# Optimization experiments

Hardware: AMD Instinct MI355X
Metric: run time of the kernel (lower is better)

Reference implementation:

```python
import jax, jax.numpy as jnp
import numpy as np
from jax import lax

NUM_GROUP = 512
GROUP_SIZE = 32


def fps(xyz, npoint):
    """Farthest point sampling. xyz: [B, N, 3] -> centers [B, npoint, 3]."""
    B, N, _ = xyz.shape
    big = jnp.asarray(1e10, xyz.dtype)

    def body(carry, _):
        min_d, farthest = carry  # [B, N], [B]
        centroid = jnp.take_along_axis(xyz, farthest[:, None, None], axis=1)  # [B,1,3]
        d = jnp.sum((xyz - centroid) ** 2, axis=-1)  # [B, N]
        min_d = jnp.minimum(min_d, d)
        nxt = jnp.argmax(min_d, axis=-1).astype(jnp.int32)
        return (min_d, nxt), farthest

    init = (jnp.full((B, N), big, xyz.dtype), jnp.zeros((B,), jnp.int32))
    _, idxs = lax.scan(body, init, None, length=npoint)  # [npoint, B]
    idxs = idxs.T  # [B, npoint]
    return jnp.take_along_axis(xyz, idxs[..., None], axis=1)  # [B, npoint, 3]


def knn_idx(xyz, center, k):
    """xyz [B,N,3], center [B,G,3] -> idx [B,G,k] of k nearest (squared L2)."""
    # [B, G, N] squared distances
    d2 = jnp.sum((center[:, :, None, :] - xyz[:, None, :, :]) ** 2, axis=-1)
    _, idx = lax.top_k(-d2, k)  # smallest distances
    return idx


def setup_inputs() -> dict:
    key = jax.random.key(0)
    xyz = jax.random.normal(key, (32, 3, 8192), dtype=jnp.float32)
    return {"xyz": xyz}


def reference(xyz):
    # xyz: [B, 3, N] -> [B, N, 3]
    pts = jnp.transpose(xyz, (0, 2, 1))[:, :, :3]
    B, N, _ = pts.shape
    center = fps(pts, NUM_GROUP)                  # [B, G, 3]
    idx = knn_idx(pts, center, GROUP_SIZE)        # [B, G, k]
    flat_idx = idx.reshape(B, NUM_GROUP * GROUP_SIZE)
    neighborhood = jnp.take_along_axis(pts, flat_idx[..., None], axis=1)
    neighborhood = neighborhood.reshape(B, NUM_GROUP, GROUP_SIZE, 3)
    neighborhood = neighborhood - center[:, :, None, :]
    return neighborhood, center
```

## Files before the change

kernel.cpp:

```cpp
#include <hip/hip_runtime.h>

typedef unsigned long long u64;
typedef unsigned int u32;
typedef float v2f __attribute__((ext_vector_type(2)));

#define BATCH 32
#define NPTS  8192
#define NGRP  512
#define KNN_K 32

#define FPS_T 256
#define FPS_W (FPS_T / 64)
#define PPAIR (NPTS / FPS_T / 2)
#define KNN_WPB 4
#define QCAP 128

__device__ __forceinline__ float sq3(float dx, float dy, float dz) {
    return __fadd_rn(__fadd_rn(__fmul_rn(dx, dx), __fmul_rn(dy, dy)), __fmul_rn(dz, dz));
}

__device__ __forceinline__ u64 packdi(float d, int n) {
    return ((u64)__float_as_uint(d) << 32) | (u32)n;
}

__device__ __forceinline__ u64 umin64(u64 a, u64 b) { return a < b ? a : b; }
__device__ __forceinline__ u64 umax64(u64 a, u64 b) { return a > b ? a : b; }

__device__ __forceinline__ u64 shfl_xor_u64(u64 v, int m) {
    int lo = __shfl_xor((int)(u32)v, m, 64);
    int hi = __shfl_xor((int)(u32)(v >> 32), m, 64);
    return ((u64)(u32)hi << 32) | (u32)lo;
}

__device__ __forceinline__ u64 shfl_u64(u64 v, int src) {
    int lo = __shfl((int)(u32)v, src, 64);
    int hi = __shfl((int)(u32)(v >> 32), src, 64);
    return ((u64)(u32)hi << 32) | (u32)lo;
}

template <int CTRL>
__device__ __forceinline__ u64 dpp_max_step(u64 k) {
    u32 plo = (u32)__builtin_amdgcn_update_dpp(0, (int)(u32)k, CTRL, 0xF, 0xF, true);
    u32 phi = (u32)__builtin_amdgcn_update_dpp(0, (int)(u32)(k >> 32), CTRL, 0xF, 0xF, true);
    u64 p = ((u64)phi << 32) | plo;
    return k > p ? k : p;
}
__device__ __forceinline__ u64 dpp_wave_max(u64 k) {
    k = dpp_max_step<0x111>(k);
    k = dpp_max_step<0x112>(k);
    k = dpp_max_step<0x114>(k);
    k = dpp_max_step<0x118>(k);
    k = dpp_max_step<0x142>(k);
    k = dpp_max_step<0x143>(k);
    return k;
}

__device__ __forceinline__ u64 lane_sort64(u64 v, int lane) {
#pragma unroll
    for (int k = 2; k <= 64; k <<= 1) {
#pragma unroll
        for (int j = k >> 1; j > 0; j >>= 1) {
            u64 p = shfl_xor_u64(v, j);
            bool keepmin = (((lane & k) == 0) == ((lane & j) == 0));
            u64 mn = umin64(v, p), mx = umax64(v, p);
            v = keepmin ? mn : mx;
        }
    }
    return v;
}

__device__ __forceinline__ u64 lane_merge64(u64 m, u64 c, int lane) {
    u64 cr = shfl_xor_u64(c, 63);
    u64 z = umin64(m, cr);
#pragma unroll
    for (int dd = 32; dd > 0; dd >>= 1) {
        u64 p = shfl_xor_u64(z, dd);
        u64 mn = umin64(z, p), mx = umax64(z, p);
        z = (lane & dd) ? mx : mn;
    }
    return z;
}

__device__ __forceinline__ void knn_step(u64& m, u64& tau, int& cnt, u64* sbuf,
                                         float x, float y, float z,
                                         float cx, float cy, float cz,
                                         int n, int lane) {
    float d = sq3(__fsub_rn(x, cx), __fsub_rn(y, cy), __fsub_rn(z, cz));
    u64 kk = packdi(d, n);
    bool cand = kk < tau;
    u64 mask = __ballot(cand);
    if (mask) {
        u32 below = __builtin_amdgcn_mbcnt_hi(
            (u32)(mask >> 32), __builtin_amdgcn_mbcnt_lo((u32)mask, 0));
        if (cand) sbuf[cnt + below] = kk;
        cnt += (int)__popcll(mask);
        if (cnt >= 64) {
            u64 c = sbuf[lane];
            c = lane_sort64(c, lane);
            m = lane_merge64(m, c, lane);
            tau = shfl_u64(m, 31);
            int rem = cnt - 64;
            if (lane < rem) sbuf[lane] = sbuf[64 + lane];
            cnt = rem;
        }
    }
}

__global__ __launch_bounds__(FPS_T) void fps_kernel(const float* __restrict__ in,
                                                    float* __restrict__ centers) {
#pragma clang fp contract(off)
    __shared__ float sx[NPTS];
    __shared__ float sy[NPTS];
    __shared__ float sz[NPTS];
    __shared__ u64 s_key[2][FPS_W];
    __shared__ float s_out[NGRP * 3];

    const int b = blockIdx.x;
    const int t = threadIdx.x;
    const int w = t >> 6;
    const float* xp = in + (size_t)b * 3 * NPTS;
    const float* yp = xp + NPTS;
    const float* zp = xp + 2 * NPTS;

    v2f xr[PPAIR], yr[PPAIR], zr[PPAIR], md[PPAIR];
#pragma unroll
    for (int i = 0; i < PPAIR; ++i) {
        int n = i * (2 * FPS_T) + 2 * t;
        xr[i] = *(const v2f*)(xp + n);
        yr[i] = *(const v2f*)(yp + n);
        zr[i] = *(const v2f*)(zp + n);
        *(v2f*)(sx + n) = xr[i];
        *(v2f*)(sy + n) = yr[i];
        *(v2f*)(sz + n) = zr[i];
        md[i] = (v2f){1e10f, 1e10f};
    }
    __syncthreads();

    int cur = 0;
    for (int r = 0; r < NGRP; ++r) {
        const float cx = sx[cur], cy = sy[cur], cz = sz[cur];
        if (t == 0) {
            s_out[r * 3 + 0] = cx;
            s_out[r * 3 + 1] = cy;
            s_out[r * 3 + 2] = cz;
        }

        float bd0 = -1.0f, bd1 = -1.0f;
        int   bi0 = 0,     bi1 = 0;
#pragma unroll
        for (int i = 0; i < PPAIR; ++i) {
            v2f dx = xr[i] - cx;
            v2f dy = yr[i] - cy;
            v2f dz = zr[i] - cz;
            v2f dd = dx * dx + dy * dy + dz * dz;
            md[i] = __builtin_elementwise_min(md[i], dd);
            int n = i * (2 * FPS_T) + 2 * t;
            if (md[i].x > bd0) { bd0 = md[i].x; bi0 = n; }
            if (md[i].y > bd1) { bd1 = md[i].y; bi1 = n + 1; }
        }
        u64 k0 = ((u64)__float_as_uint(bd0) << 32) | (u32)(~(u32)bi0);
        u64 k1 = ((u64)__float_as_uint(bd1) << 32) | (u32)(~(u32)bi1);
        u64 k = dpp_wave_max(umax64(k0, k1));
        if ((t & 63) == 63) s_key[r & 1][w] = k;
        __syncthreads();
        u64 m = umax64(umax64(s_key[r & 1][0], s_key[r & 1][1]),
                       umax64(s_key[r & 1][2], s_key[r & 1][3]));
        cur = (int)(~(u32)m);
    }

    __syncthreads();
    float* cdst = centers + (size_t)b * NGRP * 3;
    for (int i = t; i < NGRP * 3; i += FPS_T) cdst[i] = s_out[i];
}

__global__ __launch_bounds__(KNN_WPB * 64) void knn_kernel(const float* __restrict__ in,
                                                           const float* __restrict__ centers,
                                                           float* __restrict__ out) {
    __shared__ u64 sbuf[KNN_WPB][QCAP];

    const int wave = threadIdx.x >> 6;
    const int lane = threadIdx.x & 63;
    const int cid  = blockIdx.x * KNN_WPB + wave;
    const int b    = cid >> 9;

    const float* xp = in + (size_t)b * 3 * NPTS;
    const float* yp = xp + NPTS;
    const float* zp = xp + 2 * NPTS;

    const float cx = centers[cid * 3 + 0];
    const float cy = centers[cid * 3 + 1];
    const float cz = centers[cid * 3 + 2];

    float x = xp[lane], y = yp[lane], z = zp[lane];
    u64 m = packdi(sq3(__fsub_rn(x, cx), __fsub_rn(y, cy), __fsub_rn(z, cz)), lane);
    m = lane_sort64(m, lane);
    u64 tau = shfl_u64(m, 31);
    int cnt = 0;

    int j = 1;
#pragma unroll 1
    for (; j + 3 < NPTS / 64; j += 4) {
        int n0 = j * 64 + lane, n1 = n0 + 64, n2 = n0 + 128, n3 = n0 + 192;
        float x0 = xp[n0], y0 = yp[n0], z0 = zp[n0];
        float x1 = xp[n1], y1 = yp[n1], z1 = zp[n1];
        float x2 = xp[n2], y2 = yp[n2], z2 = zp[n2];
        float x3 = xp[n3], y3 = yp[n3], z3 = zp[n3];
        knn_step(m, tau, cnt, sbuf[wave], x0, y0, z0, cx, cy, cz, n0, lane);
        knn_step(m, tau, cnt, sbuf[wave], x1, y1, z1, cx, cy, cz, n1, lane);
        knn_step(m, tau, cnt, sbuf[wave], x2, y2, z2, cx, cy, cz, n2, lane);
        knn_step(m, tau, cnt, sbuf[wave], x3, y3, z3, cx, cy, cz, n3, lane);
    }
    for (; j < NPTS / 64; ++j) {
        int n = j * 64 + lane;
        knn_step(m, tau, cnt, sbuf[wave], xp[n], yp[n], zp[n], cx, cy, cz, n, lane);
    }
    while (cnt > 0) {
        int take = cnt < 64 ? cnt : 64;
        u64 v = sbuf[wave][lane];
        u64 c = (lane < take) ? v : ~0ull;
        c = lane_sort64(c, lane);
        m = lane_merge64(m, c, lane);
        int rem = cnt - take;
        if (lane < rem) sbuf[wave][lane] = sbuf[wave][64 + lane];
        cnt = rem;
    }

    if (lane < KNN_K) {
        int n = (int)(u32)m;
        size_t o = (size_t)cid * (KNN_K * 3) + (size_t)lane * 3;
        out[o + 0] = __fsub_rn(xp[n], cx);
        out[o + 1] = __fsub_rn(yp[n], cy);
        out[o + 2] = __fsub_rn(zp[n], cz);
    }
}

extern "C" void kernel_launch(void* const* d_in, const int* in_sizes, int n_in,
                              void* d_out, int out_size, void* d_ws, size_t ws_size,
                              hipStream_t stream) {
    const float* in  = (const float*)d_in[0];
    float* out       = (float*)d_out;
    float* centers   = out + (size_t)BATCH * NGRP * KNN_K * 3;

    fps_kernel<<<BATCH, FPS_T, 0, stream>>>(in, centers);
    knn_kernel<<<(BATCH * NGRP) / KNN_WPB, KNN_WPB * 64, 0, stream>>>(in, centers, out);
}
```

Baseline: 568.2 us.

## Stage KNN point tiles into LDS with double-buffered async global-to-LDS loads

The KNN kernel now stages 1024-point xyz tiles into shared memory using global_load_lds and double buffers them, so all waves in a block share a single load of each tile. Before, every wave read the full point cloud from global memory on its own. Waves per block rise from 4 to 8, which is valid because every block's centers belong to the same batch. The cost is a block-wide barrier after each tile, which ties divergent per-wave merge work together. The change also relies on the barrier waiting for the asynchronous LDS loads to complete.

Result: slower. 582.4 us (+2.5%).

```diff
diff --git a/kernel.cpp b/kernel.cpp
--- a/kernel.cpp
+++ b/kernel.cpp
@@ -12,8 +12,14 @@
 #define FPS_T 256
 #define FPS_W (FPS_T / 64)
 #define PPAIR (NPTS / FPS_T / 2)
-#define KNN_WPB 4
-#define QCAP 128
+
+#define KNN_WPB 8
+#define KNN_T   (KNN_WPB * 64)
+#define QCAP    128
+#define TP      1024
+#define NT      (NPTS / TP)
+#define NCOL    (TP / 64)
+#define NCHUNK  (3 * TP / 256)
 
 __device__ __forceinline__ float sq3(float dx, float dy, float dz) {
     return __fadd_rn(__fadd_rn(__fmul_rn(dx, dx), __fmul_rn(dy, dy)), __fmul_rn(dz, dz));
@@ -173,9 +179,24 @@
     for (int i = t; i < NGRP * 3; i += FPS_T) cdst[i] = s_out[i];
 }
 
-__global__ __launch_bounds__(KNN_WPB * 64) void knn_kernel(const float* __restrict__ in,
-                                                           const float* __restrict__ centers,
-                                                           float* __restrict__ out) {
+__device__ __forceinline__ void stage_tile(const float* __restrict__ xp,
+                                           float (*dst)[TP], int t,
+                                           int wave, int lane) {
+    for (int c = wave; c < NCHUNK; c += KNN_WPB) {
+        const int plane = c >> 2;
+        const int off = (c & 3) << 8;
+        const float* gs = xp + (size_t)plane * NPTS + t * TP + off + lane * 4;
+        __builtin_amdgcn_global_load_lds(
+            (const __attribute__((address_space(1))) void*)gs,
+            (__attribute__((address_space(3))) void*)&dst[plane][off],
+            16, 0, 0);
+    }
+}
+
+__global__ __launch_bounds__(KNN_T) void knn_kernel(const float* __restrict__ in,
+                                                    const float* __restrict__ centers,
+                                                    float* __restrict__ out) {
+    __shared__ float stg[2][3][TP];
     __shared__ u64 sbuf[KNN_WPB][QCAP];
 
     const int wave = threadIdx.x >> 6;
@@ -191,29 +212,42 @@
     const float cy = centers[cid * 3 + 1];
     const float cz = centers[cid * 3 + 2];
 
-    float x = xp[lane], y = yp[lane], z = zp[lane];
-    u64 m = packdi(sq3(__fsub_rn(x, cx), __fsub_rn(y, cy), __fsub_rn(z, cz)), lane);
+    stage_tile(xp, stg[0], 0, wave, lane);
+    __syncthreads();
+
+    float xs = stg[0][0][lane], ys = stg[0][1][lane], zs = stg[0][2][lane];
+    u64 m = packdi(sq3(__fsub_rn(xs, cx), __fsub_rn(ys, cy), __fsub_rn(zs, cz)), lane);
     m = lane_sort64(m, lane);
     u64 tau = shfl_u64(m, 31);
     int cnt = 0;
 
-    int j = 1;
 #pragma unroll 1
-    for (; j + 3 < NPTS / 64; j += 4) {
-        int n0 = j * 64 + lane, n1 = n0 + 64, n2 = n0 + 128, n3 = n0 + 192;
-        float x0 = xp[n0], y0 = yp[n0], z0 = zp[n0];
-        float x1 = xp[n1], y1 = yp[n1], z1 = zp[n1];
-        float x2 = xp[n2], y2 = yp[n2], z2 = zp[n2];
-        float x3 = xp[n3], y3 = yp[n3], z3 = zp[n3];
-        knn_step(m, tau, cnt, sbuf[wave], x0, y0, z0, cx, cy, cz, n0, lane);
-        knn_step(m, tau, cnt, sbuf[wave], x1, y1, z1, cx, cy, cz, n1, lane);
-        knn_step(m, tau, cnt, sbuf[wave], x2, y2, z2, cx, cy, cz, n2, lane);
-        knn_step(m, tau, cnt, sbuf[wave], x3, y3, z3, cx, cy, cz, n3, lane);
-    }
-    for (; j < NPTS / 64; ++j) {
-        int n = j * 64 + lane;
-        knn_step(m, tau, cnt, sbuf[wave], xp[n], yp[n], zp[n], cx, cy, cz, n, lane);
-    }
+    for (int t = 0; t < NT; ++t) {
+        if (t + 1 < NT) stage_tile(xp, stg[(t + 1) & 1], t + 1, wave, lane);
+        const float* bx = stg[t & 1][0];
+        const float* by = stg[t & 1][1];
+        const float* bz = stg[t & 1][2];
+        const int base = t * TP;
+        int j = (t == 0) ? 1 : 0;
+#pragma unroll 1
+        for (; j + 3 < NCOL; j += 4) {
+            int p0 = j * 64 + lane, p1 = p0 + 64, p2 = p0 + 128, p3 = p0 + 192;
+            float x0 = bx[p0], y0 = by[p0], z0 = bz[p0];
+            float x1 = bx[p1], y1 = by[p1], z1 = bz[p1];
+            float x2 = bx[p2], y2 = by[p2], z2 = bz[p2];
+            float x3 = bx[p3], y3 = by[p3], z3 = bz[p3];
+            knn_step(m, tau, cnt, sbuf[wave], x0, y0, z0, cx, cy, cz, base + p0, lane);
+            knn_step(m, tau, cnt, sbuf[wave], x1, y1, z1, cx, cy, cz, base + p1, lane);
+            knn_step(m, tau, cnt, sbuf[wave], x2, y2, z2, cx, cy, cz, base + p2, lane);
+            knn_step(m, tau, cnt, sbuf[wave], x3, y3, z3, cx, cy, cz, base + p3, lane);
+        }
+        for (; j < NCOL; ++j) {
+            int p = j * 64 + lane;
+            knn_step(m, tau, cnt, sbuf[wave], bx[p], by[p], bz[p], cx, cy, cz, base + p, lane);
+        }
+        __syncthreads();
+    }
+
     while (cnt > 0) {
         int take = cnt < 64 ? cnt : 64;
         u64 v = sbuf[wave][lane];
@@ -242,5 +276,5 @@
     float* centers   = out + (size_t)BATCH * NGRP * KNN_K * 3;
 
     fps_kernel<<<BATCH, FPS_T, 0, stream>>>(in, centers);
-    knn_kernel<<<(BATCH * NGRP) / KNN_WPB, KNN_WPB * 64, 0, stream>>>(in, centers, out);
-}
+    knn_kernel<<<(BATCH * NGRP) / KNN_WPB, KNN_T, 0, stream>>>(in, centers, out);
+}
```

## Sort points by Morton grid cell and prune KNN chunks with bounding boxes

Applied to the files above, without the earlier changes.

Adds a build kernel that bins each batch's points into a 16^3 grid, orders them by Morton code, and writes the sorted coordinates, original indices and per-64-point-chunk bounding boxes to workspace. The KNN kernel visits chunks nearest-first by box lower bound and stops once that bound exceeds the current 32nd-best distance, instead of scanning all 8192 points. This aims to cut most of the distance evaluations and candidate merges. In exchange it adds an extra launch, workspace traffic, a per-chunk wave reduction, and a 0.999 slack factor in the early-exit test. A brute-force fallback is kept for when the workspace is too small.

New measurement: 557.7 us. About the same (-1.8%).

```diff
diff --git a/kernel.cpp b/kernel.cpp
--- a/kernel.cpp
+++ b/kernel.cpp
@@ -12,8 +12,17 @@
 #define FPS_T 256
 #define FPS_W (FPS_T / 64)
 #define PPAIR (NPTS / FPS_T / 2)
-#define KNN_WPB 4
-#define QCAP 128
+
+#define KNN_WPB 8
+#define KNN_T   (KNN_WPB * 64)
+#define QCAP    128
+
+#define NCH     (NPTS / 64)
+#define GC      16
+#define NCELL   (GC * GC * GC)
+#define BT      512
+#define BPT     (NPTS / BT)
+#define WSF     (4 * NPTS + NCH * 6)
 
 __device__ __forceinline__ float sq3(float dx, float dy, float dz) {
     return __fadd_rn(__fadd_rn(__fmul_rn(dx, dx), __fmul_rn(dy, dy)), __fmul_rn(dz, dz));
@@ -173,14 +182,207 @@
     for (int i = t; i < NGRP * 3; i += FPS_T) cdst[i] = s_out[i];
 }
 
-__global__ __launch_bounds__(KNN_WPB * 64) void knn_kernel(const float* __restrict__ in,
-                                                           const float* __restrict__ centers,
-                                                           float* __restrict__ out) {
+__device__ __forceinline__ int cell_of(float v) {
+    int c = (int)((v + 4.0f) * 2.0f);
+    c = c < 0 ? 0 : c;
+    return c > (GC - 1) ? (GC - 1) : c;
+}
+__device__ __forceinline__ u32 part3_4(u32 v) {
+    return (v & 1u) | ((v & 2u) << 2) | ((v & 4u) << 4) | ((v & 8u) << 6);
+}
+
+__global__ __launch_bounds__(BT) void build_kernel(const float* __restrict__ in,
+                                                   float* __restrict__ ws) {
+    __shared__ u32 hist[NCELL];
+    __shared__ float sxl[NPTS];
+    __shared__ float syl[NPTS];
+    __shared__ float szl[NPTS];
+    __shared__ u32 wtot[BT / 64];
+
+    const int b = blockIdx.x;
+    const int t = threadIdx.x;
+    const int lane = t & 63;
+    const int w = t >> 6;
+    const float* xp = in + (size_t)b * 3 * NPTS;
+    const float* yp = xp + NPTS;
+    const float* zp = xp + 2 * NPTS;
+    float* wsb = ws + (size_t)b * WSF;
+    float* ws_sx = wsb;
+    float* ws_sy = wsb + NPTS;
+    float* ws_sz = wsb + 2 * NPTS;
+    u32*   ws_si = (u32*)(wsb + 3 * NPTS);
+    float* ws_ab = wsb + 4 * NPTS;
+
+    for (int i = t; i < NCELL; i += BT) hist[i] = 0;
+    __syncthreads();
+
+    float px[BPT], py[BPT], pz[BPT];
+    int pc[BPT];
+#pragma unroll
+    for (int i = 0; i < BPT; ++i) {
+        int n = i * BT + t;
+        float x = xp[n], y = yp[n], z = zp[n];
+        px[i] = x; py[i] = y; pz[i] = z;
+        pc[i] = (int)(part3_4((u32)cell_of(x)) | (part3_4((u32)cell_of(y)) << 1) |
+                      (part3_4((u32)cell_of(z)) << 2));
+        atomicAdd(&hist[pc[i]], 1u);
+    }
+    __syncthreads();
+
+    u32 h[NCELL / BT];
+    u32 lsum = 0;
+#pragma unroll
+    for (int j = 0; j < NCELL / BT; ++j) { h[j] = hist[t * (NCELL / BT) + j]; lsum += h[j]; }
+    u32 x = lsum;
+#pragma unroll
+    for (int d = 1; d < 64; d <<= 1) {
+        u32 y = __shfl_up(x, d, 64);
+        if (lane >= d) x += y;
+    }
+    if (lane == 63) wtot[w] = x;
+    u32 wexcl = x - lsum;
+    __syncthreads();
+    u32 base = 0;
+    for (int j = 0; j < w; ++j) base += wtot[j];
+    u32 run = base + wexcl;
+#pragma unroll
+    for (int j = 0; j < NCELL / BT; ++j) {
+        u32 c = h[j];
+        hist[t * (NCELL / BT) + j] = run;
+        run += c;
+    }
+    __syncthreads();
+
+#pragma unroll
+    for (int i = 0; i < BPT; ++i) {
+        u32 pos = atomicAdd(&hist[pc[i]], 1u);
+        sxl[pos] = px[i]; syl[pos] = py[i]; szl[pos] = pz[i];
+        ws_si[pos] = (u32)(i * BT + t);
+    }
+    __syncthreads();
+
+    for (int i = t; i < NPTS; i += BT) {
+        ws_sx[i] = sxl[i]; ws_sy[i] = syl[i]; ws_sz[i] = szl[i];
+    }
+    for (int q = w; q < NCH; q += BT / 64) {
+        int p = q * 64 + lane;
+        float X = sxl[p], Y = syl[p], Z = szl[p];
+        float xlo = X, xhi = X, ylo = Y, yhi = Y, zlo = Z, zhi = Z;
+#pragma unroll
+        for (int d = 1; d < 64; d <<= 1) {
+            xlo = fminf(xlo, __shfl_xor(xlo, d, 64)); xhi = fmaxf(xhi, __shfl_xor(xhi, d, 64));
+            ylo = fminf(ylo, __shfl_xor(ylo, d, 64)); yhi = fmaxf(yhi, __shfl_xor(yhi, d, 64));
+            zlo = fminf(zlo, __shfl_xor(zlo, d, 64)); zhi = fmaxf(zhi, __shfl_xor(zhi, d, 64));
+        }
+        if (lane == 0) {
+            float* a = ws_ab + q * 6;
+            a[0] = xlo; a[1] = xhi; a[2] = ylo; a[3] = yhi; a[4] = zlo; a[5] = zhi;
+        }
+    }
+}
+
+__global__ __launch_bounds__(KNN_T) void knn_kernel(const float* __restrict__ in,
+                                                    const float* __restrict__ centers,
+                                                    const float* __restrict__ ws,
+                                                    float* __restrict__ out) {
+    __shared__ float s_ab[NCH * 6];
     __shared__ u64 sbuf[KNN_WPB][QCAP];
 
     const int wave = threadIdx.x >> 6;
     const int lane = threadIdx.x & 63;
     const int cid  = blockIdx.x * KNN_WPB + wave;
+    const int b    = cid >> 9;
+
+    const float* xp = in + (size_t)b * 3 * NPTS;
+    const float* yp = xp + NPTS;
+    const float* zp = xp + 2 * NPTS;
+    const float* wsb = ws + (size_t)b * WSF;
+    const float* sxs = wsb;
+    const float* sys = wsb + NPTS;
+    const float* szs = wsb + 2 * NPTS;
+    const u32*   sidx = (const u32*)(wsb + 3 * NPTS);
+    const float* ab = wsb + 4 * NPTS;
+
+    for (int i = threadIdx.x; i < NCH * 6; i += KNN_T) s_ab[i] = ab[i];
+    __syncthreads();
+
+    const float cx = centers[cid * 3 + 0];
+    const float cy = centers[cid * 3 + 1];
+    const float cz = centers[cid * 3 + 2];
+
+    u64 k0, k1;
+    {
+        const float* a0 = &s_ab[lane * 6];
+        float dx = fmaxf(fmaxf(__fsub_rn(a0[0], cx), __fsub_rn(cx, a0[1])), 0.0f);
+        float dy = fmaxf(fmaxf(__fsub_rn(a0[2], cy), __fsub_rn(cy, a0[3])), 0.0f);
+        float dz = fmaxf(fmaxf(__fsub_rn(a0[4], cz), __fsub_rn(cz, a0[5])), 0.0f);
+        k0 = ((u64)__float_as_uint(dx * dx + dy * dy + dz * dz) << 32) | (u32)lane;
+        const float* a1 = &s_ab[(lane + 64) * 6];
+        dx = fmaxf(fmaxf(__fsub_rn(a1[0], cx), __fsub_rn(cx, a1[1])), 0.0f);
+        dy = fmaxf(fmaxf(__fsub_rn(a1[2], cy), __fsub_rn(cy, a1[3])), 0.0f);
+        dz = fmaxf(fmaxf(__fsub_rn(a1[4], cz), __fsub_rn(cz, a1[5])), 0.0f);
+        k1 = ((u64)__float_as_uint(dx * dx + dy * dy + dz * dz) << 32) | (u32)(lane + 64);
+    }
+
+    u64 m, tau;
+    int cnt = 0;
+
+    {
+        u64 inv = dpp_wave_max(~umin64(k0, k1));
+        u64 got = ~shfl_u64(inv, 63);
+        int c = (int)(u32)got;
+        int p = c * 64 + lane;
+        float X = sxs[p], Y = sys[p], Z = szs[p];
+        int n = (int)sidx[p];
+        m = lane_sort64(packdi(sq3(__fsub_rn(X, cx), __fsub_rn(Y, cy), __fsub_rn(Z, cz)), n),
+                        lane);
+        tau = shfl_u64(m, 31);
+        if (lane == (c & 63)) { if (c < 64) k0 = ~0ull; else k1 = ~0ull; }
+    }
+
+    for (int it = 1; it < NCH; ++it) {
+        u64 inv = dpp_wave_max(~umin64(k0, k1));
+        u64 got = ~shfl_u64(inv, 63);
+        float lb = __uint_as_float((u32)(got >> 32));
+        float tau_d = __uint_as_float((u32)(tau >> 32));
+        if (lb * 0.999f > tau_d) break;
+        int c = (int)(u32)got;
+        int p = c * 64 + lane;
+        float X = sxs[p], Y = sys[p], Z = szs[p];
+        int n = (int)sidx[p];
+        knn_step(m, tau, cnt, sbuf[wave], X, Y, Z, cx, cy, cz, n, lane);
+        if (lane == (c & 63)) { if (c < 64) k0 = ~0ull; else k1 = ~0ull; }
+    }
+
+    while (cnt > 0) {
+        int take = cnt < 64 ? cnt : 64;
+        u64 v = sbuf[wave][lane];
+        u64 c = (lane < take) ? v : ~0ull;
+        c = lane_sort64(c, lane);
+        m = lane_merge64(m, c, lane);
+        int rem = cnt - take;
+        if (lane < rem) sbuf[wave][lane] = sbuf[wave][64 + lane];
+        cnt = rem;
+    }
+
+    if (lane < KNN_K) {
+        int n = (int)(u32)m;
+        size_t o = (size_t)cid * (KNN_K * 3) + (size_t)lane * 3;
+        out[o + 0] = __fsub_rn(xp[n], cx);
+        out[o + 1] = __fsub_rn(yp[n], cy);
+        out[o + 2] = __fsub_rn(zp[n], cz);
+    }
+}
+
+#define KNN_WPB_FB 4
+__global__ __launch_bounds__(KNN_WPB_FB * 64) void knn_fallback(
+    const float* __restrict__ in, const float* __restrict__ centers,
+    float* __restrict__ out) {
+    __shared__ u64 sbuf[KNN_WPB_FB][QCAP];
+
+    const int wave = threadIdx.x >> 6;
+    const int lane = threadIdx.x & 63;
+    const int cid  = blockIdx.x * KNN_WPB_FB + wave;
     const int b    = cid >> 9;
 
     const float* xp = in + (size_t)b * 3 * NPTS;
@@ -224,7 +426,6 @@
         if (lane < rem) sbuf[wave][lane] = sbuf[wave][64 + lane];
         cnt = rem;
     }
-
     if (lane < KNN_K) {
         int n = (int)(u32)m;
         size_t o = (size_t)cid * (KNN_K * 3) + (size_t)lane * 3;
@@ -241,6 +442,15 @@
     float* out       = (float*)d_out;
     float* centers   = out + (size_t)BATCH * NGRP * KNN_K * 3;
 
+    const size_t need = (size_t)BATCH * WSF * sizeof(float);
+
     fps_kernel<<<BATCH, FPS_T, 0, stream>>>(in, centers);
-    knn_kernel<<<(BATCH * NGRP) / KNN_WPB, KNN_WPB * 64, 0, stream>>>(in, centers, out);
-}
+    if (d_ws != nullptr && ws_size >= need) {
+        build_kernel<<<BATCH, BT, 0, stream>>>(in, (float*)d_ws);
+        knn_kernel<<<(BATCH * NGRP) / KNN_WPB, KNN_T, 0, stream>>>(
+            in, centers, (const float*)d_ws, out);
+    } else {
+        knn_fallback<<<(BATCH * NGRP) / KNN_WPB_FB, KNN_WPB_FB * 64, 0, stream>>>(
+            in, centers, out);
+    }
+}
```
